# Optimization experiments

Hardware: AMD Instinct MI355X
Metric: run time of the kernel (lower is better)

Reference implementation:

```python
import jax, jax.numpy as jnp
import numpy as np

B, T, C, H = 4, 2048, 1024, 16
D = C // H          # head dim = 64
W_FF = 4 * C        # 4096
EPS = 1e-5


def layernorm(x, w, b):
    mu = jnp.mean(x, axis=-1, keepdims=True)
    var = jnp.mean(jnp.square(x - mu), axis=-1, keepdims=True)
    return (x - mu) / jnp.sqrt(var + EPS) * w + b


def setup_inputs() -> dict:
    key = jax.random.key(0)
    ks = jax.random.split(key, 12)
    s_attn = 1.0 / np.sqrt(C)
    s_ff1 = 1.0 / np.sqrt(C)
    s_ff2 = 1.0 / np.sqrt(W_FF)
    return {
        "x": jax.random.normal(ks[0], (B, T, C), jnp.float32),
        "ln1_w": jnp.ones((C,), jnp.float32),
        "ln1_b": jnp.zeros((C,), jnp.float32),
        # weights stored [in, out] (transpose of torch Linear.weight)
        "Wq": jax.random.normal(ks[1], (C, C), jnp.float32) * s_attn,
        "bq": jnp.zeros((C,), jnp.float32),
        "Wk": jax.random.normal(ks[2], (C, C), jnp.float32) * s_attn,
        "bk": jnp.zeros((C,), jnp.float32),
        "Wv": jax.random.normal(ks[3], (C, C), jnp.float32) * s_attn,
        "bv": jnp.zeros((C,), jnp.float32),
        "Wo": jax.random.normal(ks[4], (C, C), jnp.float32) * s_attn,
        "bo": jnp.zeros((C,), jnp.float32),
        "ln2_w": jnp.ones((C,), jnp.float32),
        "ln2_b": jnp.zeros((C,), jnp.float32),
        "W1": jax.random.normal(ks[5], (C, W_FF), jnp.float32) * s_ff1,
        "b1": jnp.zeros((W_FF,), jnp.float32),
        "W2": jax.random.normal(ks[6], (W_FF, C), jnp.float32) * s_ff2,
        "b2": jnp.zeros((C,), jnp.float32),
    }


def reference(x, ln1_w, ln1_b, Wq, bq, Wk, bk, Wv, bv, Wo, bo,
              ln2_w, ln2_b, W1, b1, W2, b2):
    b, t, c = x.shape
    # --- attention branch ---
    h = layernorm(x, ln1_w, ln1_b)
    q = (h @ Wq + bq).reshape(b, t, H, D)
    k = (h @ Wk + bk).reshape(b, t, H, D)
    v = (h @ Wv + bv).reshape(b, t, H, D)
    att = jnp.einsum("bqhd,bkhd->bhqk", q, k) / jnp.sqrt(jnp.float32(D))
    causal = jnp.tril(jnp.ones((t, t), bool))
    att = jnp.where(causal, att, -jnp.inf)
    p = jax.nn.softmax(att, axis=-1)
    y = jnp.einsum("bhqk,bkhd->bqhd", p, v).reshape(b, t, c)
    x = x + y @ Wo + bo
    # --- MLP branch (depth=2: one hidden relu layer) ---
    h2 = layernorm(x, ln2_w, ln2_b)
    x = x + jax.nn.relu(h2 @ W1 + b1) @ W2 + b2
    return x
```

## Files before the change

### kernel.cpp

```cpp
#include <hip/hip_runtime.h>
#include <cstdint>
#include <cstddef>

typedef unsigned short u16;
typedef __attribute__((ext_vector_type(8))) short bf16x8;
typedef __attribute__((ext_vector_type(4))) float f32x4;
typedef __attribute__((ext_vector_type(16))) float f32x16;
typedef __attribute__((ext_vector_type(4))) unsigned short u16x4;

#define DEV static __device__ __forceinline__

DEV u16 f2bf(float f) {
  union { float f; uint32_t u; } c; c.f = f;
  uint32_t u = c.u;
  return (u16)((u + 0x7fffu + ((u >> 16) & 1u)) >> 16);
}

DEV void gload16(const void* g, void* l) {
  __builtin_amdgcn_global_load_lds((const __attribute__((address_space(1))) void*)g,
                                   (__attribute__((address_space(3))) void*)l, 16, 0, 0);
}

__global__ __launch_bounds__(256)
void wconv_kernel(const float* __restrict__ W, u16* __restrict__ Wt, int K, int N,
                  float scale) {
  __shared__ float tile[32][33];
  const int k0 = blockIdx.y << 5;
  const int n0 = blockIdx.x << 5;
  const int c  = threadIdx.x & 31;
  const int r0 = threadIdx.x >> 5;
#pragma unroll
  for (int i = 0; i < 4; i++) {
    int r = r0 + i * 8;
    tile[r][c] = W[(size_t)(k0 + r) * N + n0 + c];
  }
  __syncthreads();
#pragma unroll
  for (int i = 0; i < 4; i++) {
    int r = r0 + i * 8;
    Wt[(size_t)(n0 + r) * K + k0 + c] = f2bf(tile[c][r] * scale);
  }
}

__global__ void bcat_kernel(const float* __restrict__ bq, const float* __restrict__ bk,
                            const float* __restrict__ bv, float* __restrict__ o,
                            float sc) {
  int i = blockIdx.x * 256 + threadIdx.x;
  float v = (i < 1024) ? bq[i] * sc : (i < 2048 ? bk[i - 1024] : bv[i - 2048]);
  o[i] = v;
}

__global__ __launch_bounds__(256)
void ln_kernel(const float* __restrict__ x, const float* __restrict__ w,
               const float* __restrict__ b, u16* __restrict__ out) {
  const int row = blockIdx.x;
  const int t = threadIdx.x;
  __shared__ float red[4];
  const float4 v = ((const float4*)(x + (size_t)row * 1024))[t];
  float s = v.x + v.y + v.z + v.w;
#pragma unroll
  for (int off = 32; off; off >>= 1) s += __shfl_xor(s, off);
  if ((t & 63) == 0) red[t >> 6] = s;
  __syncthreads();
  const float mu = (red[0] + red[1] + red[2] + red[3]) * (1.0f / 1024.0f);
  __syncthreads();
  float dx = v.x - mu, dy = v.y - mu, dz = v.z - mu, dw = v.w - mu;
  float ss = dx * dx + dy * dy + dz * dz + dw * dw;
#pragma unroll
  for (int off = 32; off; off >>= 1) ss += __shfl_xor(ss, off);
  if ((t & 63) == 0) red[t >> 6] = ss;
  __syncthreads();
  const float var = (red[0] + red[1] + red[2] + red[3]) * (1.0f / 1024.0f);
  const float rstd = rsqrtf(var + 1e-5f);
  const float4 wv = ((const float4*)w)[t];
  const float4 bv = ((const float4*)b)[t];
  u16x4 o;
  o[0] = f2bf(dx * rstd * wv.x + bv.x);
  o[1] = f2bf(dy * rstd * wv.y + bv.y);
  o[2] = f2bf(dz * rstd * wv.z + bv.z);
  o[3] = f2bf(dw * rstd * wv.w + bv.w);
  *((u16x4*)(out + (size_t)row * 1024 + t * 4)) = o;
}

template <bool RELU, bool RESID>
__global__ __launch_bounds__(256, 2)
void gemm_kernel(const u16* __restrict__ A, const u16* __restrict__ Bt,
                 const float* __restrict__ bias, const float* __restrict__ resid,
                 u16* __restrict__ outb, float* __restrict__ outf,
                 int M, int N, int K) {
  __shared__ short As[128 * 64];
  __shared__ short Bs[128 * 64];
  const int l = threadIdx.x & 63;
  const int w = threadIdx.x >> 6;
  const int m0 = blockIdx.y * 128;
  const int n0 = blockIdx.x * 128;
  const int mw = (w >> 1) * 64;
  const int nw = (w & 1) * 64;

  f32x4 acc[4][4];
#pragma unroll
  for (int i = 0; i < 4; i++)
#pragma unroll
    for (int j = 0; j < 4; j++) acc[i][j] = {0.f, 0.f, 0.f, 0.f};

  const int nk = K >> 6;
  for (int kt = 0; kt < nk; ++kt) {
    const int k0 = kt << 6;
#pragma unroll
    for (int i = 0; i < 4; i++) {
      int o = ((w * 4 + i) << 10) + l * 16;
      int row = o >> 7;
      int ke = (o & 127) >> 1;
      gload16(A + (size_t)(m0 + row) * K + k0 + ke, (short*)As + ((w * 4 + i) << 9));
      gload16(Bt + (size_t)(n0 + row) * K + k0 + ke, (short*)Bs + ((w * 4 + i) << 9));
    }
    __syncthreads();
#pragma unroll
    for (int kg = 0; kg < 2; ++kg) {
      bf16x8 af[4], bfr[4];
#pragma unroll
      for (int i = 0; i < 4; i++) {
        af[i]  = *(const bf16x8*)(As + (mw + i * 16 + (l & 15)) * 64 + kg * 32 + (l >> 4) * 8);
        bfr[i] = *(const bf16x8*)(Bs + (nw + i * 16 + (l & 15)) * 64 + kg * 32 + (l >> 4) * 8);
      }
#pragma unroll
      for (int i = 0; i < 4; i++)
#pragma unroll
        for (int j = 0; j < 4; j++)
          acc[i][j] = __builtin_amdgcn_mfma_f32_16x16x32_bf16(af[i], bfr[j], acc[i][j], 0, 0, 0);
    }
    __syncthreads();
  }

#pragma unroll
  for (int i = 0; i < 4; i++) {
    const int r0 = m0 + mw + i * 16 + ((l >> 4) << 2);
#pragma unroll
    for (int j = 0; j < 4; j++) {
      const int c = n0 + nw + j * 16 + (l & 15);
      const float bb = bias[c];
#pragma unroll
      for (int r = 0; r < 4; r++) {
        float v = acc[i][j][r] + bb;
        if (RELU) v = fmaxf(v, 0.0f);
        const size_t idx = (size_t)(r0 + r) * N + c;
        if (RESID)
          outf[idx] = resid[idx] + v;
        else
          outb[idx] = f2bf(v);
      }
    }
  }
}

__global__ __launch_bounds__(256)
void vtrans_kernel(const u16* __restrict__ QKV, u16* __restrict__ Vt_g) {
  __shared__ u16 tile[32][33];
  const int t0 = blockIdx.x * 32;
  const int d0 = blockIdx.y * 32;
  const int bh = blockIdx.z;
  const int bb = bh >> 4, hh = bh & 15;
  const int c = threadIdx.x & 31, r0 = threadIdx.x >> 5;
#pragma unroll
  for (int i = 0; i < 4; i++) {
    int r = r0 + i * 8;
    tile[r][c] = QKV[(size_t)(bb * 2048 + t0 + r) * 3072 + 2048 + hh * 64 + d0 + c];
  }
  __syncthreads();
#pragma unroll
  for (int i = 0; i < 4; i++) {
    int r = r0 + i * 8;
    Vt_g[((size_t)bh * 64 + d0 + r) * 2048 + t0 + c] = tile[c][r];
  }
}

__global__ __launch_bounds__(128, 2)
void attn_kernel(const u16* __restrict__ QKV, const u16* __restrict__ Vt_g,
                 u16* __restrict__ Y) {
  __shared__ short Ks[2][64 * 64];
  __shared__ short Vs[2][64 * 64];
  const int tid = threadIdx.x;
  const int l = tid & 63;
  const int w = tid >> 6;
  const int lane31 = l & 31;
  const int khalf = l >> 5;
  const int qt = gridDim.x - 1 - blockIdx.x;
  const int bh = blockIdx.y;
  const int bb = bh >> 4, hh = bh & 15;
  const size_t baseT = (size_t)bb * 2048;
  const int qrel = qt * 64 + w * 32 + lane31;
  const size_t qrow = baseT + qrel;

  bf16x8 qf[4];
  {
    const u16* qp = QKV + qrow * 3072 + hh * 64 + khalf * 8;
#pragma unroll
    for (int s = 0; s < 4; s++) qf[s] = *(const bf16x8*)(qp + s * 16);
  }

  f32x16 yac0, yac1;
#pragma unroll
  for (int i = 0; i < 16; i++) { yac0[i] = 0.f; yac1[i] = 0.f; }
  float m_ = -INFINITY, s_ = 0.f;

  auto stage = [&](int j, int buf) {
    const u16* kb = QKV + (baseT + j * 64) * 3072 + 1024 + hh * 64;
    const u16* vb = Vt_g + (size_t)bh * 64 * 2048 + j * 64;
#pragma unroll
    for (int i = 0; i < 4; i++) {
      int idx = i * 128 + tid;
      int row = idx >> 3, cb = idx & 7;
      int cbs = (cb ^ (row & 7)) * 8;
      gload16(kb + (size_t)row * 3072 + cbs, &Ks[buf][(i * 128 + w * 64) * 8]);
      gload16(vb + (size_t)row * 2048 + cbs, &Vs[buf][(i * 128 + w * 64) * 8]);
    }
  };

  const int jmax = qt;
  stage(0, 0);
  __syncthreads();
  int cur = 0;
  for (int j = 0; j <= jmax; ++j) {
    if (j < jmax) stage(j + 1, cur ^ 1);
    const short* Kc = Ks[cur];
    const short* Vc = Vs[cur];

    f32x16 sa0, sa1;
#pragma unroll
    for (int i = 0; i < 16; i++) { sa0[i] = 0.f; sa1[i] = 0.f; }
    __builtin_amdgcn_s_setprio(1);
#pragma unroll
    for (int s = 0; s < 4; s++) {
      int cb = ((s * 2 + khalf) ^ (l & 7)) * 8;
      bf16x8 k0 = *(const bf16x8*)(Kc + lane31 * 64 + cb);
      bf16x8 k1 = *(const bf16x8*)(Kc + (32 + lane31) * 64 + cb);
      sa0 = __builtin_amdgcn_mfma_f32_32x32x16_bf16(k0, qf[s], sa0, 0, 0, 0);
      sa1 = __builtin_amdgcn_mfma_f32_32x32x16_bf16(k1, qf[s], sa1, 0, 0, 0);
    }
    __builtin_amdgcn_s_setprio(0);

    float p0[16], p1[16];
    float tmax = -INFINITY;
    const bool bnd = (j == qt);
#pragma unroll
    for (int r = 0; r < 16; r++) {
      float v0 = sa0[r], v1 = sa1[r];
      if (bnd) {
        int kg = j * 64 + 4 * khalf + (r & 3) + 8 * (r >> 2);
        if (kg > qrel) v0 = -INFINITY;
        if (kg + 32 > qrel) v1 = -INFINITY;
      }
      p0[r] = v0; p1[r] = v1;
      tmax = fmaxf(tmax, fmaxf(v0, v1));
    }
    tmax = fmaxf(tmax, __shfl_xor(tmax, 32));
    if (!__all(tmax - m_ <= 8.0f)) {
      const float nm = fmaxf(m_, tmax);
      const float alpha = exp2f(m_ - nm);
      m_ = nm;
      s_ *= alpha;
#pragma unroll
      for (int i = 0; i < 16; i++) { yac0[i] *= alpha; yac1[i] *= alpha; }
    }
    float sum = 0.f;
#pragma unroll
    for (int r = 0; r < 16; r++) {
      p0[r] = exp2f(p0[r] - m_);
      p1[r] = exp2f(p1[r] - m_);
      sum += p0[r] + p1[r];
    }
    sum += __shfl_xor(sum, 32);
    s_ += sum;

    uint32_t pk0[8], pk1[8];
#pragma unroll
    for (int jj = 0; jj < 4; jj++) {
      int rb = 4 * jj;
      uint32_t a, b;
      asm("v_cvt_pk_bf16_f32 %0, %1, %2" : "=v"(a) : "v"(p0[rb]), "v"(p0[rb + 1]));
      asm("v_cvt_pk_bf16_f32 %0, %1, %2" : "=v"(b) : "v"(p0[rb + 2]), "v"(p0[rb + 3]));
      pk0[jj] = a; pk1[jj] = b;
    }
#pragma unroll
    for (int jj = 0; jj < 4; jj++) {
      int rb = 4 * jj;
      uint32_t a, b;
      asm("v_cvt_pk_bf16_f32 %0, %1, %2" : "=v"(a) : "v"(p1[rb]), "v"(p1[rb + 1]));
      asm("v_cvt_pk_bf16_f32 %0, %1, %2" : "=v"(b) : "v"(p1[rb + 2]), "v"(p1[rb + 3]));
      pk0[4 + jj] = a; pk1[4 + jj] = b;
    }

#pragma unroll
    for (int kvs = 0; kvs < 4; kvs++) {
      uint32_t x0 = pk0[2 * kvs], y0 = pk0[2 * kvs + 1];
      uint32_t x1 = pk1[2 * kvs], y1 = pk1[2 * kvs + 1];
      asm volatile("v_permlane32_swap_b32 %0, %1" : "+v"(x0), "+v"(y0));
      asm volatile("v_permlane32_swap_b32 %0, %1" : "+v"(x1), "+v"(y1));
      union { uint32_t u[4]; bf16x8 v; } pf;
      pf.u[0] = x0; pf.u[1] = x1; pf.u[2] = y0; pf.u[3] = y1;
      int cb = ((kvs * 2 + khalf) ^ (l & 7)) * 8;
      bf16x8 v0 = *(const bf16x8*)(Vc + lane31 * 64 + cb);
      bf16x8 v1 = *(const bf16x8*)(Vc + (32 + lane31) * 64 + cb);
      __builtin_amdgcn_s_setprio(1);
      yac0 = __builtin_amdgcn_mfma_f32_32x32x16_bf16(v0, pf.v, yac0, 0, 0, 0);
      yac1 = __builtin_amdgcn_mfma_f32_32x32x16_bf16(v1, pf.v, yac1, 0, 0, 0);
      __builtin_amdgcn_s_setprio(0);
    }
    __syncthreads();
    cur ^= 1;
  }

  const float sinv = 1.0f / s_;
  u16* yp = Y + qrow * 1024 + hh * 64;
#pragma unroll
  for (int rq = 0; rq < 4; rq++) {
    u16x4 o0, o1;
#pragma unroll
    for (int e = 0; e < 4; e++) {
      o0[e] = f2bf(yac0[rq * 4 + e] * sinv);
      o1[e] = f2bf(yac1[rq * 4 + e] * sinv);
    }
    *(u16x4*)(yp + 8 * rq + 4 * khalf) = o0;
    *(u16x4*)(yp + 32 + 8 * rq + 4 * khalf) = o1;
  }
}

extern "C" void kernel_launch(void* const* d_in, const int* in_sizes, int n_in,
                              void* d_out, int out_size, void* d_ws, size_t ws_size,
                              hipStream_t stream) {
  const float* x    = (const float*)d_in[0];
  const float* ln1w = (const float*)d_in[1];
  const float* ln1b = (const float*)d_in[2];
  const float* Wq   = (const float*)d_in[3];
  const float* bq   = (const float*)d_in[4];
  const float* Wk   = (const float*)d_in[5];
  const float* bk   = (const float*)d_in[6];
  const float* Wv   = (const float*)d_in[7];
  const float* bv   = (const float*)d_in[8];
  const float* Wo   = (const float*)d_in[9];
  const float* bo   = (const float*)d_in[10];
  const float* ln2w = (const float*)d_in[11];
  const float* ln2b = (const float*)d_in[12];
  const float* W1   = (const float*)d_in[13];
  const float* b1   = (const float*)d_in[14];
  const float* W2   = (const float*)d_in[15];
  const float* b2   = (const float*)d_in[16];
  float* out = (float*)d_out;
  char* ws = (char*)d_ws;
  const size_t MB = 1ull << 20;
  const float SC = 0.125f * 1.44269504088896340736f;

  u16* h     = (u16*)(ws);
  u16* qkv   = (u16*)(ws + 16 * MB);
  u16* ff1   = (u16*)(ws);
  u16* Vt_g  = (u16*)(ws + 64 * MB);
  float* x1  = (float*)(ws + 64 * MB);
  u16* y     = (u16*)(ws + 96 * MB);
  u16* Wqkvt = (u16*)(ws + 112 * MB);
  u16* Wot   = (u16*)(ws + 118 * MB);
  u16* W1t   = (u16*)(ws + 120 * MB);
  u16* W2t   = (u16*)(ws + 128 * MB);
  float* bqkv = (float*)(ws + 136 * MB);

  dim3 tb(256);
  wconv_kernel<<<dim3(32, 32), tb, 0, stream>>>(Wq, Wqkvt, 1024, 1024, SC);
  wconv_kernel<<<dim3(32, 32), tb, 0, stream>>>(Wk, Wqkvt + (1024u * 1024), 1024, 1024, 1.0f);
  wconv_kernel<<<dim3(32, 32), tb, 0, stream>>>(Wv, Wqkvt + (2048u * 1024), 1024, 1024, 1.0f);
  wconv_kernel<<<dim3(32, 32), tb, 0, stream>>>(Wo, Wot, 1024, 1024, 1.0f);
  wconv_kernel<<<dim3(128, 32), tb, 0, stream>>>(W1, W1t, 1024, 4096, 1.0f);
  wconv_kernel<<<dim3(32, 128), tb, 0, stream>>>(W2, W2t, 4096, 1024, 1.0f);
  bcat_kernel<<<dim3(12), tb, 0, stream>>>(bq, bk, bv, bqkv, SC);

  ln_kernel<<<8192, tb, 0, stream>>>(x, ln1w, ln1b, h);

  gemm_kernel<false, false><<<dim3(24, 64), tb, 0, stream>>>(h, Wqkvt, bqkv, nullptr, qkv, nullptr, 8192, 3072, 1024);

  vtrans_kernel<<<dim3(64, 2, 64), tb, 0, stream>>>(qkv, Vt_g);

  attn_kernel<<<dim3(32, 64), dim3(128), 0, stream>>>(qkv, Vt_g, y);

  gemm_kernel<false, true><<<dim3(8, 64), tb, 0, stream>>>(y, Wot, bo, x, nullptr, x1, 8192, 1024, 1024);

  ln_kernel<<<8192, tb, 0, stream>>>(x1, ln2w, ln2b, y);

  gemm_kernel<true, false><<<dim3(32, 64), tb, 0, stream>>>(y, W1t, b1, nullptr, ff1, nullptr, 8192, 4096, 1024);

  gemm_kernel<false, true><<<dim3(8, 64), tb, 0, stream>>>(ff1, W2t, b2, x1, nullptr, out, 8192, 1024, 4096);
}
```

Measured before the change: 622.7 us.

## Pack K/V into contiguous tiles and use 256-query attention blocks with XCD-aware mapping

Adds a K repack kernel and changes the V transpose so each 64-key tile of K and V is contiguous per head. The attention kernel now uses 512-thread blocks covering 256 queries (8 waves), so each K/V tile loaded into LDS is shared by four times as many queries. The grid is flattened with a mapping that places each head's query tiles on the same XCD. Waves whose queries lie entirely before a key tile skip its compute but still take part in staging and barriers, which adds idle imbalance on the causal diagonal, and the extra K pack pass adds traffic.

```diff
diff --git a/kernel.cpp b/kernel.cpp
--- a/kernel.cpp
+++ b/kernel.cpp
@@ -154,7 +154,18 @@
 }
 
 __global__ __launch_bounds__(256)
-void vtrans_kernel(const u16* __restrict__ QKV, u16* __restrict__ Vt_g) {
+void kpack_kernel(const u16* __restrict__ QKV, u16* __restrict__ Kp) {
+  const int id = blockIdx.x * 256 + threadIdx.x;
+  const int d8 = id & 7;
+  const int t  = (id >> 3) & 2047;
+  const int bh = id >> 14;
+  const int bb = bh >> 4, hh = bh & 15;
+  const bf16x8 v = *(const bf16x8*)(QKV + (size_t)(bb * 2048 + t) * 3072 + 1024 + hh * 64 + d8 * 8);
+  *(bf16x8*)(Kp + ((size_t)bh * 2048 + t) * 64 + d8 * 8) = v;
+}
+
+__global__ __launch_bounds__(256)
+void vpack_kernel(const u16* __restrict__ QKV, u16* __restrict__ Vp) {
   __shared__ u16 tile[32][33];
   const int t0 = blockIdx.x * 32;
   const int d0 = blockIdx.y * 32;
@@ -170,13 +181,13 @@
 #pragma unroll
   for (int i = 0; i < 4; i++) {
     int r = r0 + i * 8;
-    Vt_g[((size_t)bh * 64 + d0 + r) * 2048 + t0 + c] = tile[c][r];
-  }
-}
-
-__global__ __launch_bounds__(128, 2)
-void attn_kernel(const u16* __restrict__ QKV, const u16* __restrict__ Vt_g,
-                 u16* __restrict__ Y) {
+    Vp[(((size_t)bh * 32 + (t0 >> 6)) * 64 + d0 + r) * 64 + (t0 & 63) + c] = tile[c][r];
+  }
+}
+
+__global__ __launch_bounds__(512, 4)
+void attn_kernel(const u16* __restrict__ QKV, const u16* __restrict__ Kp,
+                 const u16* __restrict__ Vp, u16* __restrict__ Y) {
   __shared__ short Ks[2][64 * 64];
   __shared__ short Vs[2][64 * 64];
   const int tid = threadIdx.x;
@@ -184,19 +195,26 @@
   const int w = tid >> 6;
   const int lane31 = l & 31;
   const int khalf = l >> 5;
-  const int qt = gridDim.x - 1 - blockIdx.x;
-  const int bh = blockIdx.y;
+  const int id = blockIdx.x;
+  const int xcd = id & 7, s = id >> 3;
+  const int bh = xcd * 8 + (s & 7);
+  const int qt = 7 - (s >> 3);
   const int bb = bh >> 4, hh = bh & 15;
   const size_t baseT = (size_t)bb * 2048;
-  const int qrel = qt * 64 + w * 32 + lane31;
+  const int qrel = qt * 256 + w * 32 + lane31;
   const size_t qrow = baseT + qrel;
+  const int wave_qmin = qt * 256 + w * 32;
+  const int myqmax = wave_qmin + 31;
 
   bf16x8 qf[4];
   {
     const u16* qp = QKV + qrow * 3072 + hh * 64 + khalf * 8;
 #pragma unroll
-    for (int s = 0; s < 4; s++) qf[s] = *(const bf16x8*)(qp + s * 16);
-  }
+    for (int si = 0; si < 4; si++) qf[si] = *(const bf16x8*)(qp + si * 16);
+  }
+
+  const u16* KpB = Kp + (size_t)bh * 131072;
+  const u16* VpB = Vp + (size_t)bh * 131072;
 
   f32x16 yac0, yac1;
 #pragma unroll
@@ -204,107 +222,104 @@
   float m_ = -INFINITY, s_ = 0.f;
 
   auto stage = [&](int j, int buf) {
-    const u16* kb = QKV + (baseT + j * 64) * 3072 + 1024 + hh * 64;
-    const u16* vb = Vt_g + (size_t)bh * 64 * 2048 + j * 64;
-#pragma unroll
-    for (int i = 0; i < 4; i++) {
-      int idx = i * 128 + tid;
-      int row = idx >> 3, cb = idx & 7;
-      int cbs = (cb ^ (row & 7)) * 8;
-      gload16(kb + (size_t)row * 3072 + cbs, &Ks[buf][(i * 128 + w * 64) * 8]);
-      gload16(vb + (size_t)row * 2048 + cbs, &Vs[buf][(i * 128 + w * 64) * 8]);
-    }
+    const int row = tid >> 3, cb = tid & 7;
+    const int cbs = (cb ^ (row & 7)) * 8;
+    const size_t toff = (size_t)j * 4096;
+    gload16(KpB + toff + row * 64 + cbs, &Ks[buf][(w * 64) * 8]);
+    gload16(VpB + toff + row * 64 + cbs, &Vs[buf][(w * 64) * 8]);
   };
 
-  const int jmax = qt;
+  const int jmax = 4 * qt + 3;
   stage(0, 0);
   __syncthreads();
   int cur = 0;
   for (int j = 0; j <= jmax; ++j) {
     if (j < jmax) stage(j + 1, cur ^ 1);
-    const short* Kc = Ks[cur];
-    const short* Vc = Vs[cur];
-
-    f32x16 sa0, sa1;
-#pragma unroll
-    for (int i = 0; i < 16; i++) { sa0[i] = 0.f; sa1[i] = 0.f; }
-    __builtin_amdgcn_s_setprio(1);
-#pragma unroll
-    for (int s = 0; s < 4; s++) {
-      int cb = ((s * 2 + khalf) ^ (l & 7)) * 8;
-      bf16x8 k0 = *(const bf16x8*)(Kc + lane31 * 64 + cb);
-      bf16x8 k1 = *(const bf16x8*)(Kc + (32 + lane31) * 64 + cb);
-      sa0 = __builtin_amdgcn_mfma_f32_32x32x16_bf16(k0, qf[s], sa0, 0, 0, 0);
-      sa1 = __builtin_amdgcn_mfma_f32_32x32x16_bf16(k1, qf[s], sa1, 0, 0, 0);
-    }
-    __builtin_amdgcn_s_setprio(0);
-
-    float p0[16], p1[16];
-    float tmax = -INFINITY;
-    const bool bnd = (j == qt);
-#pragma unroll
-    for (int r = 0; r < 16; r++) {
-      float v0 = sa0[r], v1 = sa1[r];
-      if (bnd) {
-        int kg = j * 64 + 4 * khalf + (r & 3) + 8 * (r >> 2);
-        if (kg > qrel) v0 = -INFINITY;
-        if (kg + 32 > qrel) v1 = -INFINITY;
-      }
-      p0[r] = v0; p1[r] = v1;
-      tmax = fmaxf(tmax, fmaxf(v0, v1));
-    }
-    tmax = fmaxf(tmax, __shfl_xor(tmax, 32));
-    if (!__all(tmax - m_ <= 8.0f)) {
-      const float nm = fmaxf(m_, tmax);
-      const float alpha = exp2f(m_ - nm);
-      m_ = nm;
-      s_ *= alpha;
-#pragma unroll
-      for (int i = 0; i < 16; i++) { yac0[i] *= alpha; yac1[i] *= alpha; }
-    }
-    float sum = 0.f;
-#pragma unroll
-    for (int r = 0; r < 16; r++) {
-      p0[r] = exp2f(p0[r] - m_);
-      p1[r] = exp2f(p1[r] - m_);
-      sum += p0[r] + p1[r];
-    }
-    sum += __shfl_xor(sum, 32);
-    s_ += sum;
-
-    uint32_t pk0[8], pk1[8];
-#pragma unroll
-    for (int jj = 0; jj < 4; jj++) {
-      int rb = 4 * jj;
-      uint32_t a, b;
-      asm("v_cvt_pk_bf16_f32 %0, %1, %2" : "=v"(a) : "v"(p0[rb]), "v"(p0[rb + 1]));
-      asm("v_cvt_pk_bf16_f32 %0, %1, %2" : "=v"(b) : "v"(p0[rb + 2]), "v"(p0[rb + 3]));
-      pk0[jj] = a; pk1[jj] = b;
-    }
-#pragma unroll
-    for (int jj = 0; jj < 4; jj++) {
-      int rb = 4 * jj;
-      uint32_t a, b;
-      asm("v_cvt_pk_bf16_f32 %0, %1, %2" : "=v"(a) : "v"(p1[rb]), "v"(p1[rb + 1]));
-      asm("v_cvt_pk_bf16_f32 %0, %1, %2" : "=v"(b) : "v"(p1[rb + 2]), "v"(p1[rb + 3]));
-      pk0[4 + jj] = a; pk1[4 + jj] = b;
-    }
-
-#pragma unroll
-    for (int kvs = 0; kvs < 4; kvs++) {
-      uint32_t x0 = pk0[2 * kvs], y0 = pk0[2 * kvs + 1];
-      uint32_t x1 = pk1[2 * kvs], y1 = pk1[2 * kvs + 1];
-      asm volatile("v_permlane32_swap_b32 %0, %1" : "+v"(x0), "+v"(y0));
-      asm volatile("v_permlane32_swap_b32 %0, %1" : "+v"(x1), "+v"(y1));
-      union { uint32_t u[4]; bf16x8 v; } pf;
-      pf.u[0] = x0; pf.u[1] = x1; pf.u[2] = y0; pf.u[3] = y1;
-      int cb = ((kvs * 2 + khalf) ^ (l & 7)) * 8;
-      bf16x8 v0 = *(const bf16x8*)(Vc + lane31 * 64 + cb);
-      bf16x8 v1 = *(const bf16x8*)(Vc + (32 + lane31) * 64 + cb);
+    if (j * 64 <= myqmax) {
+      const short* Kc = Ks[cur];
+      const short* Vc = Vs[cur];
+
+      f32x16 sa0, sa1;
+#pragma unroll
+      for (int i = 0; i < 16; i++) { sa0[i] = 0.f; sa1[i] = 0.f; }
       __builtin_amdgcn_s_setprio(1);
-      yac0 = __builtin_amdgcn_mfma_f32_32x32x16_bf16(v0, pf.v, yac0, 0, 0, 0);
-      yac1 = __builtin_amdgcn_mfma_f32_32x32x16_bf16(v1, pf.v, yac1, 0, 0, 0);
+#pragma unroll
+      for (int si = 0; si < 4; si++) {
+        int cb = ((si * 2 + khalf) ^ (l & 7)) * 8;
+        bf16x8 k0 = *(const bf16x8*)(Kc + lane31 * 64 + cb);
+        bf16x8 k1 = *(const bf16x8*)(Kc + (32 + lane31) * 64 + cb);
+        sa0 = __builtin_amdgcn_mfma_f32_32x32x16_bf16(k0, qf[si], sa0, 0, 0, 0);
+        sa1 = __builtin_amdgcn_mfma_f32_32x32x16_bf16(k1, qf[si], sa1, 0, 0, 0);
+      }
       __builtin_amdgcn_s_setprio(0);
+
+      float p0[16], p1[16];
+      float tmax = -INFINITY;
+      const bool bnd = (j * 64 + 63 > wave_qmin);
+#pragma unroll
+      for (int r = 0; r < 16; r++) {
+        float v0 = sa0[r], v1 = sa1[r];
+        if (bnd) {
+          int kg = j * 64 + 4 * khalf + (r & 3) + 8 * (r >> 2);
+          if (kg > qrel) v0 = -INFINITY;
+          if (kg + 32 > qrel) v1 = -INFINITY;
+        }
+        p0[r] = v0; p1[r] = v1;
+        tmax = fmaxf(tmax, fmaxf(v0, v1));
+      }
+      tmax = fmaxf(tmax, __shfl_xor(tmax, 32));
+      if (!__all(tmax - m_ <= 8.0f)) {
+        const float nm = fmaxf(m_, tmax);
+        const float alpha = exp2f(m_ - nm);
+        m_ = nm;
+        s_ *= alpha;
+#pragma unroll
+        for (int i = 0; i < 16; i++) { yac0[i] *= alpha; yac1[i] *= alpha; }
+      }
+      float sum = 0.f;
+#pragma unroll
+      for (int r = 0; r < 16; r++) {
+        p0[r] = exp2f(p0[r] - m_);
+        p1[r] = exp2f(p1[r] - m_);
+        sum += p0[r] + p1[r];
+      }
+      sum += __shfl_xor(sum, 32);
+      s_ += sum;
+
+      uint32_t pk0[8], pk1[8];
+#pragma unroll
+      for (int jj = 0; jj < 4; jj++) {
+        int rb = 4 * jj;
+        uint32_t a, b;
+        asm("v_cvt_pk_bf16_f32 %0, %1, %2" : "=v"(a) : "v"(p0[rb]), "v"(p0[rb + 1]));
+        asm("v_cvt_pk_bf16_f32 %0, %1, %2" : "=v"(b) : "v"(p0[rb + 2]), "v"(p0[rb + 3]));
+        pk0[jj] = a; pk1[jj] = b;
+      }
+#pragma unroll
+      for (int jj = 0; jj < 4; jj++) {
+        int rb = 4 * jj;
+        uint32_t a, b;
+        asm("v_cvt_pk_bf16_f32 %0, %1, %2" : "=v"(a) : "v"(p1[rb]), "v"(p1[rb + 1]));
+        asm("v_cvt_pk_bf16_f32 %0, %1, %2" : "=v"(b) : "v"(p1[rb + 2]), "v"(p1[rb + 3]));
+        pk0[4 + jj] = a; pk1[4 + jj] = b;
+      }
+
+#pragma unroll
+      for (int kvs = 0; kvs < 4; kvs++) {
+        uint32_t x0 = pk0[2 * kvs], y0 = pk0[2 * kvs + 1];
+        uint32_t x1 = pk1[2 * kvs], y1 = pk1[2 * kvs + 1];
+        asm volatile("v_permlane32_swap_b32 %0, %1" : "+v"(x0), "+v"(y0));
+        asm volatile("v_permlane32_swap_b32 %0, %1" : "+v"(x1), "+v"(y1));
+        union { uint32_t u[4]; bf16x8 v; } pf;
+        pf.u[0] = x0; pf.u[1] = x1; pf.u[2] = y0; pf.u[3] = y1;
+        int cb = ((kvs * 2 + khalf) ^ (l & 7)) * 8;
+        bf16x8 v0 = *(const bf16x8*)(Vc + lane31 * 64 + cb);
+        bf16x8 v1 = *(const bf16x8*)(Vc + (32 + lane31) * 64 + cb);
+        __builtin_amdgcn_s_setprio(1);
+        yac0 = __builtin_amdgcn_mfma_f32_32x32x16_bf16(v0, pf.v, yac0, 0, 0, 0);
+        yac1 = __builtin_amdgcn_mfma_f32_32x32x16_bf16(v1, pf.v, yac1, 0, 0, 0);
+        __builtin_amdgcn_s_setprio(0);
+      }
     }
     __syncthreads();
     cur ^= 1;
@@ -353,7 +368,8 @@
   u16* h     = (u16*)(ws);
   u16* qkv   = (u16*)(ws + 16 * MB);
   u16* ff1   = (u16*)(ws);
-  u16* Vt_g  = (u16*)(ws + 64 * MB);
+  u16* Kp    = (u16*)(ws + 64 * MB);
+  u16* Vp    = (u16*)(ws + 80 * MB);
   float* x1  = (float*)(ws + 64 * MB);
   u16* y     = (u16*)(ws + 96 * MB);
   u16* Wqkvt = (u16*)(ws + 112 * MB);
@@ -375,9 +391,10 @@
 
   gemm_kernel<false, false><<<dim3(24, 64), tb, 0, stream>>>(h, Wqkvt, bqkv, nullptr, qkv, nullptr, 8192, 3072, 1024);
 
-  vtrans_kernel<<<dim3(64, 2, 64), tb, 0, stream>>>(qkv, Vt_g);
-
-  attn_kernel<<<dim3(32, 64), dim3(128), 0, stream>>>(qkv, Vt_g, y);
+  kpack_kernel<<<4096, tb, 0, stream>>>(qkv, Kp);
+  vpack_kernel<<<dim3(64, 2, 64), tb, 0, stream>>>(qkv, Vp);
+
+  attn_kernel<<<512, dim3(512), 0, stream>>>(qkv, Kp, Vp, y);
 
   gemm_kernel<false, true><<<dim3(8, 64), tb, 0, stream>>>(y, Wot, bo, x, nullptr, x1, 8192, 1024, 1024);
 
```

Measured after the change: 531.6 us. -14.6%, faster.
